# Performance work log

Hardware: AMD Instinct MI355X
Metric: run time of the kernel (lower is better)

Reference implementation:

```python
import jax, jax.numpy as jnp
import numpy as np

D_MODEL = 1024
N_HEADS = 16
HEAD_DIM = D_MODEL // N_HEADS


def _rotary_tables(seq_len, dim):
    # sin/cos tables: (seq_len, dim//2)
    pos = jnp.arange(seq_len, dtype=jnp.float32)[:, None]
    freqs = 1.0 / 10000.0 ** (jnp.arange(0, dim, 2, dtype=jnp.float32) / dim)
    angles = pos * freqs
    return jnp.sin(angles), jnp.cos(angles)


def _apply_rotary(x, sin, cos):
    # x: (B, H, N, head_dim); sin/cos: (N, head_dim//2) broadcast over B,H
    d_half = x.shape[-1] // 2
    x1, x2 = x[..., :d_half], x[..., d_half:]
    return jnp.concatenate([x1 * cos - x2 * sin, x1 * sin + x2 * cos], axis=-1)


def setup_inputs() -> dict:
    key = jax.random.key(0)
    k_x, k_q, k_k, k_v, k_o = jax.random.split(key, 5)
    B, N = 4, 2048
    scale = 1.0 / np.sqrt(D_MODEL)
    return {
        "x": jax.random.normal(k_x, (B, N, D_MODEL), dtype=jnp.float32),
        "Wq": jax.random.normal(k_q, (D_MODEL, D_MODEL), dtype=jnp.float32) * scale,
        "Wk": jax.random.normal(k_k, (D_MODEL, D_MODEL), dtype=jnp.float32) * scale,
        "Wv": jax.random.normal(k_v, (D_MODEL, D_MODEL), dtype=jnp.float32) * scale,
        "Wo": jax.random.normal(k_o, (D_MODEL, D_MODEL), dtype=jnp.float32) * scale,
    }


def reference(x, Wq, Wk, Wv, Wo):
    B, N, _ = x.shape
    # nn.Linear(d, d, bias=False): y = x @ W.T ; view+transpose -> (B, H, N, hd)
    def proj(W):
        return jnp.einsum('bnd,ed->bne', x, W).reshape(B, N, N_HEADS, HEAD_DIM).transpose(0, 2, 1, 3)

    Q, K, V = proj(Wq), proj(Wk), proj(Wv)
    sin, cos = _rotary_tables(N, HEAD_DIM)
    Q = _apply_rotary(Q, sin, cos)
    K = _apply_rotary(K, sin, cos)

    # SDPA (non-causal, dropout=0): softmax(Q K^T / sqrt(hd)) V
    scores = jnp.einsum('bhqd,bhkd->bhqk', Q, K) / jnp.sqrt(jnp.asarray(HEAD_DIM, x.dtype))
    attn = jax.nn.softmax(scores, axis=-1)
    out = jnp.einsum('bhqk,bhkd->bhqd', attn, V)  # (B, H, N, hd)
    out = out.transpose(0, 2, 1, 3).reshape(B, N, D_MODEL)
    return jnp.einsum('bnd,ed->bne', out, Wo)
```

## Files before the change

kernel.cpp:

```cpp
#include <hip/hip_runtime.h>
#include <stdint.h>

#define SEQ    2048
#define DMODEL 1024
#define NHEADS 16
#define HDIM   64
#define BATCH  4
#define MTOT   (BATCH*SEQ)

typedef __attribute__((ext_vector_type(8)))  short s16x8;
typedef __attribute__((ext_vector_type(4)))  short s16x4;
typedef __attribute__((ext_vector_type(4)))  float f32x4;
typedef __attribute__((ext_vector_type(16))) float f32x16;

#define OFF_SIN  ((size_t)0)
#define OFF_COS  ((size_t)262144)
#define OFF_XHI  ((size_t)524288)
#define OFF_WQH  ((size_t)34078720)
#define OFF_WKH  ((size_t)38273024)
#define OFF_WVH  ((size_t)42467328)
#define OFF_WOH  ((size_t)46661632)
#define OFF_QR   ((size_t)50855936)
#define OFF_KR   ((size_t)67633152)
#define OFF_VT   ((size_t)84410368)
#define OFF_AHI  ((size_t)101187584)

#define QSCALE 0.18033688011112042f

__device__ __forceinline__ uint16_t f2bf(float f){
  union{float f;uint32_t u;}v; v.f=f;
  uint32_t r=v.u+0x7fffu+((v.u>>16)&1u);
  return (uint16_t)(r>>16);
}
__device__ __forceinline__ float bf2f(uint16_t u){
  union{uint32_t u;float f;}v; v.u=((uint32_t)u)<<16; return v.f;
}

__device__ __forceinline__ void async16(void* lds, const void* g){
  __builtin_amdgcn_global_load_lds(
    (const __attribute__((address_space(1))) void*)g,
    (__attribute__((address_space(3))) void*)lds, 16, 0, 0);
}

__device__ __forceinline__ float fexp2(float x){
#if __has_builtin(__builtin_amdgcn_exp2f)
  return __builtin_amdgcn_exp2f(x);
#else
  float r; asm("v_exp_f32 %0, %1" : "=v"(r) : "v"(x)); return r;
#endif
}
__device__ __forceinline__ float frcp(float x){
#if __has_builtin(__builtin_amdgcn_rcpf)
  return __builtin_amdgcn_rcpf(x);
#else
  float r; asm("v_rcp_f32 %0, %1" : "=v"(r) : "v"(x)); return r;
#endif
}
__device__ __forceinline__ void plswap(unsigned a, unsigned b, unsigned &o0, unsigned &o1){
#if __has_builtin(__builtin_amdgcn_permlane32_swap)
  auto r = __builtin_amdgcn_permlane32_swap(a, b, false, false);
  o0 = (unsigned)r[0]; o1 = (unsigned)r[1];
#else
  unsigned ax = (unsigned)__shfl_xor((int)a, 32, 64);
  unsigned bx = (unsigned)__shfl_xor((int)b, 32, 64);
  bool hi = (threadIdx.x & 32) != 0;
  o0 = hi ? bx : a;
  o1 = hi ? b  : ax;
#endif
}

__global__ __launch_bounds__(256) void prep_k(
  const float* __restrict__ x,
  const float* __restrict__ Wq, const float* __restrict__ Wk,
  const float* __restrict__ Wv, const float* __restrict__ Wo,
  uint16_t* __restrict__ xhi, uint16_t* __restrict__ wqh, uint16_t* __restrict__ wkh,
  uint16_t* __restrict__ wvh, uint16_t* __restrict__ woh,
  float* __restrict__ st, float* __restrict__ ct)
{
  int b = blockIdx.x;
  if (b < 12288){
    const float* s; uint16_t* d; int i;
    if (b < 8192){ s = x; d = xhi; i = b*256 + threadIdx.x; }
    else {
      int wsel = (b - 8192) >> 10;
      int lb   = (b - 8192) & 1023;
      s = wsel==0? Wq : wsel==1? Wk : wsel==2? Wv : Wo;
      d = wsel==0? wqh: wsel==1? wkh: wsel==2? wvh: woh;
      i = lb*256 + threadIdx.x;
    }
    f32x4 v = *(const f32x4*)(s + (size_t)i*4);
    s16x4 vh;
    #pragma unroll
    for(int r=0;r<4;r++) vh[r] = (short)f2bf(v[r]);
    *(s16x4*)(d + (size_t)i*4) = vh;
  } else {
    int i = (b - 12288)*256 + threadIdx.x;
    int n = i>>5, j = i&31;
    float freq = powf(10000.f, -(float)j/32.f);
    float ang = (float)n*freq;
    st[i] = sinf(ang);
    ct[i] = cosf(ang);
  }
}

__device__ __forceinline__ void gemm_mainloop64(
  const uint16_t* __restrict__ A, const uint16_t* __restrict__ B,
  int m0, int e0, char* lA, char* lB, f32x4 acc[4][4])
{
  const int t = threadIdx.x;
  const int lane = t & 63;
  const int wr = t>>7, wc = (t>>6)&1;
  const int lq = lane&15, lg = lane>>4;
  const int rowA = wr*64 + lq;
  const int rowB = wc*64 + lq;

  int dbyte[4], srow[4], sbyte[4];
  #pragma unroll
  for (int s=0;s<4;s++){
    int d = s*4096 + t*16;
    int r = d>>7, c = (d>>4)&7;
    dbyte[s]=d; srow[s]=r; sbyte[s]=(c ^ (r&7))*16;
  }
  int chh[2];
  #pragma unroll
  for (int kh=0;kh<2;kh++) chh[kh] = (((kh<<2)|lg) ^ (lq&7))*16;
  const bool oddw = ((t>>6) & 1) != 0;
  const int cF = oddw ? chh[1] : chh[0];
  const int cS = oddw ? chh[0] : chh[1];

  const char* Ab = (const char*)A;
  const char* Bb = (const char*)B;

  for (int k0=0; k0<DMODEL; k0+=64){
    #pragma unroll
    for (int s=0;s<4;s++){
      async16(lA + dbyte[s], Ab + (size_t)(m0+srow[s])*2048 + k0*2 + sbyte[s]);
      async16(lB + dbyte[s], Bb + (size_t)(e0+srow[s])*2048 + k0*2 + sbyte[s]);
    }
    __syncthreads();
    #pragma unroll
    for (int ph=0; ph<2; ++ph){
      const int ch = ph ? cS : cF;
      s16x8 af[4], bfr[4];
      #pragma unroll
      for (int mi=0;mi<4;mi++) af[mi]  = *(const s16x8*)(lA + (rowA+mi*16)*128 + ch);
      #pragma unroll
      for (int ni=0;ni<4;ni++) bfr[ni] = *(const s16x8*)(lB + (rowB+ni*16)*128 + ch);
      __builtin_amdgcn_s_setprio(1);
      #pragma unroll
      for (int mi=0;mi<4;mi++){
        #pragma unroll
        for (int ni=0;ni<4;ni++)
          acc[mi][ni] = __builtin_amdgcn_mfma_f32_16x16x32_bf16(af[mi], bfr[ni], acc[mi][ni],0,0,0);
      }
      __builtin_amdgcn_s_setprio(0);
    }
    __syncthreads();
  }
}

__global__ __launch_bounds__(256) void gemm_qkv_k(
  const uint16_t* __restrict__ Xh,
  const uint16_t* __restrict__ WqH, const uint16_t* __restrict__ WkH, const uint16_t* __restrict__ WvH,
  const float* __restrict__ st, const float* __restrict__ ct,
  uint16_t* __restrict__ Qr, uint16_t* __restrict__ Kr, uint16_t* __restrict__ Vt)
{
  __shared__ char lA[128*128], lB[128*128];
  int mx = blockIdx.x;
  int m0 = (((mx & 7) << 3) | (mx >> 3)) * 128;
  int cti = blockIdx.y;
  int seg = cti>>3;
  int e0 = (cti&7)*128;
  const uint16_t* W = seg==0? WqH : (seg==1? WkH : WvH);
  f32x4 acc[4][4];
  #pragma unroll
  for(int i=0;i<4;i++){
    #pragma unroll
    for(int j=0;j<4;j++) acc[i][j] = (f32x4){0.f,0.f,0.f,0.f};
  }
  gemm_mainloop64(Xh, W, m0, e0, lA, lB, acc);

  int t=threadIdx.x, lane=t&63, lq=lane&15, lg=lane>>4;
  int wr=t>>7, wc=(t>>6)&1;
  int eb = e0 + wc*64;
  int h = eb>>6;
  int rbase = m0 + wr*64 + lg*4;
  if (seg<2){
    uint16_t* O = seg==0? Qr:Kr;
    float qs = seg==0 ? QSCALE : 1.0f;
    #pragma unroll
    for(int mi=0;mi<4;mi++){
      #pragma unroll
      for(int ni=0;ni<2;ni++){
        int j = ni*16+lq;
        #pragma unroll
        for(int r=0;r<4;r++){
          int m = rbase + mi*16 + r;
          int b = m>>11, n = m&2047;
          float sv = st[n*32+j], cv = ct[n*32+j];
          float x1 = acc[mi][ni][r], x2 = acc[mi][ni+2][r];
          size_t base = ((size_t)((b*NHEADS+h)*SEQ + n))*HDIM;
          O[base + j]      = f2bf((x1*cv - x2*sv)*qs);
          O[base + j + 32] = f2bf((x1*sv + x2*cv)*qs);
        }
      }
    }
  } else {
    #pragma unroll
    for(int mi=0;mi<4;mi++){
      #pragma unroll
      for(int ni=0;ni<4;ni++){
        int dh = ni*16+lq;
        int m = rbase + mi*16;
        int b = m>>11, n = m&2047;
        s16x4 v;
        #pragma unroll
        for(int r=0;r<4;r++) v[r] = (short)f2bf(acc[mi][ni][r]);
        *(s16x4*)(Vt + ((size_t)((b*NHEADS+h)*HDIM + dh))*SEQ + n) = v;
      }
    }
  }
}

__global__ __launch_bounds__(256) void attn_k(
  const uint16_t* __restrict__ Qr, const uint16_t* __restrict__ Kr, const uint16_t* __restrict__ Vt,
  uint16_t* __restrict__ Ah)
{
  __shared__ char lds[32768];

  int bid = blockIdx.x;
  int w = (bid & 7)*128 + (bid >> 3);
  int bh = w >> 4, qt = w & 15;
  int tid = threadIdx.x;
  int wid = tid >> 6, lane = tid & 63;
  int l31 = lane & 31, hi = lane >> 5;
  int q0 = qt*128 + wid*32;

  const uint16_t* Qb = Qr + (size_t)bh*SEQ*HDIM;
  const uint16_t* Kb = Kr + (size_t)bh*SEQ*HDIM;
  const uint16_t* Vb = Vt + (size_t)bh*HDIM*SEQ;

  s16x8 qf[4];
  #pragma unroll
  for (int sp=0; sp<4; ++sp)
    qf[sp] = *(const s16x8*)(Qb + (size_t)(q0 + l31)*HDIM + sp*16 + hi*8);

  s16x8 ones;
  #pragma unroll
  for (int j=0;j<8;j++) ones[j] = (short)0x3F80;

  f32x16 zm16;
  #pragma unroll
  for (int r=0;r<16;r++) zm16[r] = -16.0f;

  f32x16 oa[2], lacc;
  #pragma unroll
  for (int r=0;r<16;r++){ oa[0][r]=0.f; oa[1][r]=0.f; lacc[r]=0.f; }

  const int e7 = l31 & 7;
  const int rK = l31*128;
  const int kOff[4]  = { (((0+hi)^e7)<<4), (((2+hi)^e7)<<4), (((4+hi)^e7)<<4), (((6+hi)^e7)<<4) };
  const int vA0 = (((0+hi)^e7)<<4), vA1 = (((2+hi)^e7)<<4);
  const int vB0 = (((4+hi)^e7)<<4), vB1 = (((6+hi)^e7)<<4);
  const bool odd = (wid & 1) != 0;
  const int kBaseF = odd ? 4096 : 0,   kBaseS = odd ? 0 : 4096;
  const int vF0 = odd ? vB0 : vA0,     vF1 = odd ? vB1 : vA1;
  const int vS0 = odd ? vA0 : vB0,     vS1 = odd ? vA1 : vB1;

  auto STAGE = [&](int buf, int t){
    const char* Ks = (const char*)(Kb + (size_t)t*64*HDIM);
    char* dK = lds + buf*8192;
    char* dV = lds + 16384 + buf*8192;
    #pragma unroll
    for (int r=0; r<2; ++r){
      int ci = r*256 + tid;
      int sc = ci ^ ((ci>>3)&7);
      async16(dK + ci*16, Ks + sc*16);
    }
    #pragma unroll
    for (int r=0; r<2; ++r){
      int ci = r*256 + tid;
      int row = ci>>3;
      int sc = (ci&7) ^ (row&7);
      async16(dV + ci*16, (const char*)Vb + ((size_t)row*SEQ + (size_t)t*64)*2 + sc*16);
    }
  };

  auto SUBSTEP = [&](const char* bK, const char* bV, int kbase, int v0, int v1){
    s16x8 kf[4];
    #pragma unroll
    for (int sp=0; sp<4; ++sp)
      kf[sp] = *(const s16x8*)(bK + kbase + rK + kOff[sp]);
    f32x16 sacc = zm16;
    __builtin_amdgcn_s_setprio(1);
    #pragma unroll
    for (int sp=0; sp<4; ++sp)
      sacc = __builtin_amdgcn_mfma_f32_32x32x16_bf16(kf[sp], qf[sp], sacc, 0,0,0);
    __builtin_amdgcn_s_setprio(0);
    s16x8 vf[4];
    #pragma unroll
    for (int db=0; db<2; ++db){
      vf[db*2+0] = *(const s16x8*)(bV + db*4096 + rK + v0);
      vf[db*2+1] = *(const s16x8*)(bV + db*4096 + rK + v1);
    }
    float p[16];
    #pragma unroll
    for (int r=0;r<16;r++) p[r] = fexp2(sacc[r]);
    uint32_t pw[8];
    #pragma unroll
    for (int j=0;j<8;j++)
      asm("v_cvt_pk_bf16_f32 %0, %1, %2" : "=v"(pw[j]) : "v"(p[2*j]), "v"(p[2*j+1]));
    unsigned w0,w1,w2,w3, x0,x1,x2,x3;
    plswap(pw[0], pw[2], w0, w2);
    plswap(pw[1], pw[3], w1, w3);
    plswap(pw[4], pw[6], x0, x2);
    plswap(pw[5], pw[7], x1, x3);
    union { uint32_t wd[4]; s16x8 v; } pa0, pa1;
    pa0.wd[0]=w0; pa0.wd[1]=w1; pa0.wd[2]=w2; pa0.wd[3]=w3;
    pa1.wd[0]=x0; pa1.wd[1]=x1; pa1.wd[2]=x2; pa1.wd[3]=x3;
    __builtin_amdgcn_s_setprio(1);
    oa[0] = __builtin_amdgcn_mfma_f32_32x32x16_bf16(pa0.v, vf[0], oa[0], 0,0,0);
    oa[0] = __builtin_amdgcn_mfma_f32_32x32x16_bf16(pa1.v, vf[1], oa[0], 0,0,0);
    oa[1] = __builtin_amdgcn_mfma_f32_32x32x16_bf16(pa0.v, vf[2], oa[1], 0,0,0);
    oa[1] = __builtin_amdgcn_mfma_f32_32x32x16_bf16(pa1.v, vf[3], oa[1], 0,0,0);
    lacc = __builtin_amdgcn_mfma_f32_32x32x16_bf16(pa0.v, ones, lacc, 0,0,0);
    lacc = __builtin_amdgcn_mfma_f32_32x32x16_bf16(pa1.v, ones, lacc, 0,0,0);
    __builtin_amdgcn_s_setprio(0);
  };

  STAGE(0, 0);
  asm volatile("s_waitcnt vmcnt(0)" ::: "memory");
  __syncthreads();

  const int NT = SEQ/64;
  for (int t=0; t<NT; ++t){
    int cur = t & 1;
    if (t+1 < NT) STAGE(cur^1, t+1);
    const char* bK = lds + cur*8192;
    const char* bV = lds + 16384 + cur*8192;
    SUBSTEP(bK, bV, kBaseF, vF0, vF1);
    SUBSTEP(bK, bV, kBaseS, vS0, vS1);
    asm volatile("s_waitcnt vmcnt(0)" ::: "memory");
    __syncthreads();
  }

  int b = bh >> 4, h = bh & 15;
  #pragma unroll
  for (int r=0;r<16;r++){
    int q = (r&3) + 8*(r>>2) + 4*hi;
    float inv = frcp(lacc[r]);
    size_t mrow = ((size_t)(b*SEQ + q0 + q))*DMODEL + (size_t)h*HDIM + l31;
    #pragma unroll
    for (int db=0; db<2; ++db)
      Ah[mrow + db*32] = f2bf(oa[db][r]*inv);
  }
}

__global__ __launch_bounds__(256) void gemm_out_k(
  const uint16_t* __restrict__ Ahp, const uint16_t* __restrict__ WoH, float* __restrict__ C)
{
  __shared__ char lA[128*128], lB[128*128];
  int mx = blockIdx.x;
  int m0 = (((mx & 7) << 3) | (mx >> 3)) * 128;
  int e0 = blockIdx.y*128;
  f32x4 acc[4][4];
  #pragma unroll
  for(int i=0;i<4;i++){
    #pragma unroll
    for(int j=0;j<4;j++) acc[i][j] = (f32x4){0.f,0.f,0.f,0.f};
  }
  gemm_mainloop64(Ahp, WoH, m0, e0, lA, lB, acc);
  int t=threadIdx.x, lane=t&63, lq=lane&15, lg=lane>>4;
  int wr=t>>7, wc=(t>>6)&1;
  int rbase = m0 + wr*64 + lg*4;
  int cb = e0 + wc*64;
  #pragma unroll
  for(int mi=0;mi<4;mi++){
    #pragma unroll
    for(int ni=0;ni<4;ni++){
      #pragma unroll
      for(int r=0;r<4;r++)
        C[(size_t)(rbase+mi*16+r)*DMODEL + cb + ni*16 + lq] = acc[mi][ni][r];
    }
  }
}

extern "C" void kernel_launch(void* const* d_in, const int* in_sizes, int n_in,
                              void* d_out, int out_size, void* d_ws, size_t ws_size,
                              hipStream_t stream) {
  const float* x  = (const float*)d_in[0];
  const float* Wq = (const float*)d_in[1];
  const float* Wk = (const float*)d_in[2];
  const float* Wv = (const float*)d_in[3];
  const float* Wo = (const float*)d_in[4];
  float* out = (float*)d_out;
  char* ws = (char*)d_ws;

  float* sin_t = (float*)(ws + OFF_SIN);
  float* cos_t = (float*)(ws + OFF_COS);
  uint16_t* xhi = (uint16_t*)(ws + OFF_XHI);
  uint16_t* wqh = (uint16_t*)(ws + OFF_WQH);
  uint16_t* wkh = (uint16_t*)(ws + OFF_WKH);
  uint16_t* wvh = (uint16_t*)(ws + OFF_WVH);
  uint16_t* woh = (uint16_t*)(ws + OFF_WOH);
  uint16_t* Qr  = (uint16_t*)(ws + OFF_QR);
  uint16_t* Kr  = (uint16_t*)(ws + OFF_KR);
  uint16_t* Vt  = (uint16_t*)(ws + OFF_VT);
  uint16_t* ahi = (uint16_t*)(ws + OFF_AHI);

  prep_k<<<dim3(12544),dim3(256),0,stream>>>(x, Wq, Wk, Wv, Wo,
                                             xhi, wqh, wkh, wvh, woh, sin_t, cos_t);

  gemm_qkv_k<<<dim3(MTOT/128, 24),dim3(256),0,stream>>>(xhi, wqh, wkh, wvh,
                                                        sin_t, cos_t, Qr, Kr, Vt);
  attn_k<<<dim3(BATCH*NHEADS*(SEQ/128)),dim3(256),0,stream>>>(Qr, Kr, Vt, ahi);
  gemm_out_k<<<dim3(MTOT/128, 8),dim3(256),0,stream>>>(ahi, woh, out);
}
```

Measured before the change: 196.8 us.

## Split attention KV range into two halves and add a combine kernel

The attention kernel now launches twice as many blocks. Each block handles half of the key/value sequence and writes an unnormalized bf16 partial output plus its row-sum to scratch space reused from the dead x and weight buffers. A new elementwise combine kernel adds the two partials, divides by the summed denominators and writes the bf16 attention output for the output projection. The aim is more parallelism and better CU load balance. The cost is an extra kernel launch, extra global traffic for the partials, and an extra bf16 rounding step.

```diff
diff --git a/kernel.cpp b/kernel.cpp
--- a/kernel.cpp
+++ b/kernel.cpp
@@ -16,8 +16,12 @@
 #define OFF_SIN  ((size_t)0)
 #define OFF_COS  ((size_t)262144)
 #define OFF_XHI  ((size_t)524288)
+#define OFF_OP0  OFF_XHI
+#define OFF_OP1  ((size_t)17301504)
 #define OFF_WQH  ((size_t)34078720)
+#define OFF_L0   OFF_WQH
 #define OFF_WKH  ((size_t)38273024)
+#define OFF_L1   OFF_WKH
 #define OFF_WVH  ((size_t)42467328)
 #define OFF_WOH  ((size_t)46661632)
 #define OFF_QR   ((size_t)50855936)
@@ -224,21 +228,25 @@
 
 __global__ __launch_bounds__(256) void attn_k(
   const uint16_t* __restrict__ Qr, const uint16_t* __restrict__ Kr, const uint16_t* __restrict__ Vt,
-  uint16_t* __restrict__ Ah)
+  uint16_t* __restrict__ Op, float* __restrict__ Lp)
 {
   __shared__ char lds[32768];
 
   int bid = blockIdx.x;
-  int w = (bid & 7)*128 + (bid >> 3);
-  int bh = w >> 4, qt = w & 15;
+  int orig = (bid & 7)*256 + (bid >> 3);
+  int bh = orig >> 5;
+  int half = (orig >> 4) & 1;
+  int qt = orig & 15;
   int tid = threadIdx.x;
   int wid = tid >> 6, lane = tid & 63;
   int l31 = lane & 31, hi = lane >> 5;
   int q0 = qt*128 + wid*32;
 
   const uint16_t* Qb = Qr + (size_t)bh*SEQ*HDIM;
-  const uint16_t* Kb = Kr + (size_t)bh*SEQ*HDIM;
-  const uint16_t* Vb = Vt + (size_t)bh*HDIM*SEQ;
+  const uint16_t* Kb = Kr + (size_t)bh*SEQ*HDIM + (size_t)half*1024*HDIM;
+  const uint16_t* Vb = Vt + (size_t)bh*HDIM*SEQ + (size_t)half*1024;
+  uint16_t* Opart = Op + (size_t)half*8388608;
+  float*    Lpart = Lp + (size_t)half*1048576;
 
   s16x8 qf[4];
   #pragma unroll
@@ -332,7 +340,7 @@
   asm volatile("s_waitcnt vmcnt(0)" ::: "memory");
   __syncthreads();
 
-  const int NT = SEQ/64;
+  const int NT = 1024/64;
   for (int t=0; t<NT; ++t){
     int cur = t & 1;
     if (t+1 < NT) STAGE(cur^1, t+1);
@@ -348,12 +356,33 @@
   #pragma unroll
   for (int r=0;r<16;r++){
     int q = (r&3) + 8*(r>>2) + 4*hi;
-    float inv = frcp(lacc[r]);
     size_t mrow = ((size_t)(b*SEQ + q0 + q))*DMODEL + (size_t)h*HDIM + l31;
-    #pragma unroll
-    for (int db=0; db<2; ++db)
-      Ah[mrow + db*32] = f2bf(oa[db][r]*inv);
-  }
+    Opart[mrow]      = f2bf(oa[0][r]);
+    Opart[mrow + 32] = f2bf(oa[1][r]);
+    if (l31 == 0) Lpart[bh*SEQ + q0 + q] = lacc[r];
+  }
+}
+
+__global__ __launch_bounds__(256) void combine_k(
+  const uint16_t* __restrict__ O0, const uint16_t* __restrict__ O1,
+  const float* __restrict__ L0, const float* __restrict__ L1,
+  uint16_t* __restrict__ Ah)
+{
+  int i = blockIdx.x*256 + threadIdx.x;
+  size_t base = (size_t)i*8;
+  int m = i >> 7;
+  int e = (i & 127) * 8;
+  int h = e >> 6;
+  int b = m >> 11, q = m & 2047;
+  int li = ((b<<4) + h)*SEQ + q;
+  float inv = frcp(L0[li] + L1[li]);
+  s16x8 a = *(const s16x8*)(O0 + base);
+  s16x8 c = *(const s16x8*)(O1 + base);
+  s16x8 o;
+  #pragma unroll
+  for (int r=0;r<8;r++)
+    o[r] = (short)f2bf((bf2f((uint16_t)a[r]) + bf2f((uint16_t)c[r]))*inv);
+  *(s16x8*)(Ah + base) = o;
 }
 
 __global__ __launch_bounds__(256) void gemm_out_k(
@@ -407,12 +436,16 @@
   uint16_t* Kr  = (uint16_t*)(ws + OFF_KR);
   uint16_t* Vt  = (uint16_t*)(ws + OFF_VT);
   uint16_t* ahi = (uint16_t*)(ws + OFF_AHI);
+  uint16_t* op  = (uint16_t*)(ws + OFF_OP0);
+  float*    lp  = (float*)(ws + OFF_L0);
 
   prep_k<<<dim3(12544),dim3(256),0,stream>>>(x, Wq, Wk, Wv, Wo,
                                              xhi, wqh, wkh, wvh, woh, sin_t, cos_t);
 
   gemm_qkv_k<<<dim3(MTOT/128, 24),dim3(256),0,stream>>>(xhi, wqh, wkh, wvh,
                                                         sin_t, cos_t, Qr, Kr, Vt);
-  attn_k<<<dim3(BATCH*NHEADS*(SEQ/128)),dim3(256),0,stream>>>(Qr, Kr, Vt, ahi);
+  attn_k<<<dim3(BATCH*NHEADS*(SEQ/128)*2),dim3(256),0,stream>>>(Qr, Kr, Vt, op, lp);
+  combine_k<<<dim3(4096),dim3(256),0,stream>>>(op, op + (size_t)8388608,
+                                               lp, lp + (size_t)1048576, ahi);
   gemm_out_k<<<dim3(MTOT/128, 8),dim3(256),0,stream>>>(ahi, woh, out);
 }
```

After: 207.0 us. 1.05x slower.
